# Kernel tuning notes

Measured on AMD Instinct MI355X. Metric: run time of the kernel, lower is better.

## Reference

```python
import jax, jax.numpy as jnp
import numpy as np

EPS = 1e-05


def setup_inputs() -> dict:
    key = jax.random.key(0)
    k1, k2, k3, k4 = jax.random.split(key, 4)
    B, N, L, J = 1, 256, 192, 32
    n_feat_out = 128
    d2 = J * J  # 1024
    x_down = jax.random.normal(k1, (B, N, L, J), dtype=jnp.float32)
    x_down_w = jax.random.normal(k2, (B, N, L, J), dtype=jnp.float32)
    a_2 = jnp.ones((d2,), dtype=jnp.float32)
    b_2 = jnp.zeros((d2,), dtype=jnp.float32)
    # nn.Linear default init: U(-1/sqrt(fan_in), 1/sqrt(fan_in))
    bound = 1.0 / np.sqrt(d2)
    W = jax.random.uniform(k3, (d2, n_feat_out), dtype=jnp.float32, minval=-bound, maxval=bound)
    b = jax.random.uniform(k4, (n_feat_out,), dtype=jnp.float32, minval=-bound, maxval=bound)
    return {"x_down": x_down, "x_down_w": x_down_w, "a_2": a_2, "b_2": b_2, "W": W, "b": b}


def reference(x_down, x_down_w, a_2, b_2, W, b):
    B, N, L, J = x_down.shape
    # outer-product contraction over MSA dim: (B,L,L,J,J)
    pair = jnp.einsum('bnij,bnlm->biljm', x_down, x_down_w)
    pair = pair.reshape(B, L, L, J * J)
    # LayerNorm over last dim (biased variance, matching torch unbiased=False)
    mean = pair.mean(axis=-1, keepdims=True)
    var = pair.var(axis=-1, keepdims=True)
    pair = a_2 * (pair - mean) / jnp.sqrt(var + EPS) + b_2
    # Linear projection J^2 -> n_feat_out
    return pair @ W + b
```

## Files before the change

kernel.cpp:

```cpp
#include <hip/hip_runtime.h>
#include <hip/hip_bf16.h>
#include <stdint.h>

#define NN   256
#define LL   192
#define MDIM 6144
#define D2   1024
#define FF   128

typedef __bf16 bf16x8 __attribute__((ext_vector_type(8)));
typedef float  f32x4  __attribute__((ext_vector_type(4)));

#define MFMA16(a, b, c) __builtin_amdgcn_mfma_f32_16x16x32_bf16(a, b, c, 0, 0, 0)

__device__ __forceinline__ void gload_lds16(const void* g, void* l) {
  __builtin_amdgcn_global_load_lds(
      (__attribute__((address_space(1))) void*)(g),
      (__attribute__((address_space(3))) void*)(l),
      16, 0, 0);
}

static __device__ __forceinline__ unsigned short bf16_bits(float v) {
  __bf16 h = (__bf16)v;
  return __builtin_bit_cast(unsigned short, h);
}

__global__ __launch_bounds__(256)
void prep_all(const float* __restrict__ x1, const float* __restrict__ x2,
              const float* __restrict__ W, const float* __restrict__ a2,
              const float* __restrict__ b2, const float* __restrict__ bias,
              __bf16* __restrict__ At, __bf16* __restrict__ Bt,
              __bf16* __restrict__ WB, float* __restrict__ S,
              float* __restrict__ T) {
  __shared__ float tile[64][65];
  const int b = blockIdx.x;
  const int t = threadIdx.x;
  if (b < 768) {
    const float* src = (b < 384) ? x1 : x2;
    __bf16* dst = (b < 384) ? At : Bt;
    const int bb = (b < 384) ? b : b - 384;
    const int m0 = (bb % 96) * 64;
    const int k0 = (bb / 96) * 64;
    const int rr = t >> 4;
    const int cc = (t & 15) * 4;
#pragma unroll
    for (int it = 0; it < 4; ++it) {
      const int kr = rr + it * 16;
      const float4 v = *(const float4*)&src[(size_t)(k0 + kr) * MDIM + m0 + cc];
      tile[kr][cc + 0] = v.x;
      tile[kr][cc + 1] = v.y;
      tile[kr][cc + 2] = v.z;
      tile[kr][cc + 3] = v.w;
    }
    __syncthreads();
#pragma unroll
    for (int it = 0; it < 4; ++it) {
      const int mr = rr + it * 16;
      ushort4 u;
      u.x = bf16_bits(tile[cc + 0][mr]);
      u.y = bf16_bits(tile[cc + 1][mr]);
      u.z = bf16_bits(tile[cc + 2][mr]);
      u.w = bf16_bits(tile[cc + 3][mr]);
      *(ushort4*)&dst[(size_t)(m0 + mr) * NN + k0 + cc] = u;
    }
  } else {
    const int f = b - 768;
    float s = 0.f, tt = 0.f;
#pragma unroll
    for (int it = 0; it < 4; ++it) {
      const int k = t + it * 256;
      const float wv = W[(size_t)k * FF + f];
      const __bf16 wa = (__bf16)(a2[k] * wv);
      WB[(size_t)(k >> 5) * 4096 + f * 32 + ((k >> 3) & 3) * 8 + (k & 7)] = wa;
      s += (float)wa;
      tt += b2[k] * wv;
    }
#pragma unroll
    for (int off = 32; off; off >>= 1) {
      s += __shfl_xor(s, off);
      tt += __shfl_xor(tt, off);
    }
    const int wv_ = t >> 6, ln = t & 63;
    if (ln == 0) { tile[0][wv_] = s; tile[1][wv_] = tt; }
    __syncthreads();
    if (t == 0) {
      S[f] = tile[0][0] + tile[0][1] + tile[0][2] + tile[0][3];
      T[f] = tile[1][0] + tile[1][1] + tile[1][2] + tile[1][3] + bias[f];
    }
  }
}

__global__ __launch_bounds__(512, 4)
void fused10(const __bf16* __restrict__ At, const __bf16* __restrict__ Bt,
             const __bf16* __restrict__ WB, const float* __restrict__ S,
             const float* __restrict__ T, float* __restrict__ out) {
  __shared__ uint8_t lds[65536];
  __shared__ float mean_s[32], rstd_s[32];

  const int tid = threadIdx.x;
  const int w = tid >> 6;
  const int lane = tid & 63;
  const int q = lane >> 4;
  const int c = lane & 15;

  const int b = blockIdx.x;
  const int xcd = b & 7;
  const int s_ = b >> 3;
  const int bx = (xcd >> 1) * 12 + (s_ % 12);
  const int by = (xcd & 1) * 12 + (s_ / 12);
  const int m0 = bx * 128, n0 = by * 256;

  uint8_t* As = lds;
  uint8_t* Bs = lds + 16384;

  const int l8 = lane & 7;
  const int r8 = lane >> 3;
  const int gsw = l8 ^ r8;

  f32x4 acc[4][4];
#pragma unroll
  for (int i = 0; i < 4; ++i)
#pragma unroll
    for (int j = 0; j < 4; ++j)
      acc[i][j] = (f32x4){0.f, 0.f, 0.f, 0.f};

  const int mbase = (w & 1) * 64;
  const int nbase = (w >> 1) * 64;

  {
    const __bf16* gA = At + (size_t)(m0 + w * 16 + r8) * NN + gsw * 8;
    const __bf16* gB = Bt + (size_t)(n0 + w * 32 + r8) * NN + gsw * 8;
#pragma unroll 1
    for (int kb = 0; kb < 4; ++kb) {
      __syncthreads();
#pragma unroll
      for (int j = 0; j < 2; ++j)
        gload_lds16(gA + (size_t)j * 8 * NN, As + (w * 16 + j * 8) * 128);
#pragma unroll
      for (int j = 0; j < 4; ++j)
        gload_lds16(gB + (size_t)j * 8 * NN, Bs + (w * 32 + j * 8) * 128);
      __syncthreads();
#pragma unroll
      for (int ks = 0; ks < 2; ++ks) {
        const int slot = ((ks * 4 + q) ^ (lane & 7)) * 16;
        bf16x8 a[4];
#pragma unroll
        for (int t4 = 0; t4 < 4; ++t4)
          a[t4] = *(const bf16x8*)(As + (mbase + t4 * 16 + c) * 128 + slot);
#pragma unroll
        for (int tj = 0; tj < 4; ++tj) {
          const bf16x8 bfr =
              *(const bf16x8*)(Bs + (nbase + tj * 16 + c) * 128 + slot);
#pragma unroll
          for (int ti = 0; ti < 4; ++ti)
            acc[ti][tj] = MFMA16(a[ti], bfr, acc[ti][tj]);
        }
      }
      gA += 64;
      gB += 64;
    }
  }

  const int fs = w * 16;
  const __bf16* wbp = WB + (fs + c) * 32 + q * 8;
  bf16x8 pb[8];
  pb[0] = *(const bf16x8*)(wbp);
  pb[1] = *(const bf16x8*)(wbp + 4096);

  __syncthreads();

  const int i_hi = w & 1, l_hi = w >> 1;
#pragma unroll
  for (int ab = 0; ab < 2; ++ab) {
#pragma unroll
    for (int cb = 0; cb < 2; ++cb) {
      float s1 = 0.f, s2 = 0.f;
#pragma unroll
      for (int dti = 0; dti < 2; ++dti)
#pragma unroll
        for (int dtj = 0; dtj < 2; ++dtj)
#pragma unroll
          for (int reg = 0; reg < 4; ++reg) {
            const float v = acc[ab * 2 + dti][cb * 2 + dtj][reg];
            s1 += v; s2 += v * v;
          }
#pragma unroll
      for (int off = 32; off; off >>= 1) {
        s1 += __shfl_xor(s1, off);
        s2 += __shfl_xor(s2, off);
      }
      const float mean = s1 * (1.0f / 1024.0f);
      const float var = s2 * (1.0f / 1024.0f) - mean * mean;
      const float rstd = rsqrtf(var + 1e-5f);
      const int r = (i_hi * 2 + ab) * 8 + l_hi * 2 + cb;
      if (lane == 0) { mean_s[r] = mean; rstd_s[r] = rstd; }
      const int r7 = r & 7;
#pragma unroll
      for (int dti = 0; dti < 2; ++dti)
#pragma unroll
        for (int dtj = 0; dtj < 2; ++dtj)
#pragma unroll
          for (int rp = 0; rp < 4; rp += 2) {
            const float x = acc[ab * 2 + dti][cb * 2 + dtj][rp];
            const float y = acc[ab * 2 + dti][cb * 2 + dtj][rp + 1];
            const float send = (c & 1) ? x : y;
            const float recv = __shfl_xor(send, 1);
            const float vlo = (c & 1) ? recv : x;
            const float vhi = (c & 1) ? y : recv;
            const int reg_w = (c & 1) ? rp + 1 : rp;
            const int j = dti * 16 + q * 4 + reg_w;
            const int mm0 = dtj * 16 + (c & ~1);
            const int k = j * 32 + mm0;
            const int g = k >> 3;
            const int G = g ^ (g >> 4) ^ r7;
            const uint32_t dw =
                ((uint32_t)bf16_bits(vhi) << 16) | (uint32_t)bf16_bits(vlo);
            *(uint32_t*)(lds + r * 2048 + G * 16 + (mm0 & 7) * 2) = dw;
          }
    }
  }

  __syncthreads();
  __builtin_amdgcn_sched_barrier(0);

#pragma unroll
  for (int p = 2; p < 8; ++p)
    pb[p] = *(const bf16x8*)(wbp + p * 4096);

  f32x4 acc2[2];
  acc2[0] = (f32x4){0.f, 0.f, 0.f, 0.f};
  acc2[1] = (f32x4){0.f, 0.f, 0.f, 0.f};
  const int c7 = c & 7;
#pragma unroll
  for (int kstep = 0; kstep < 32; ++kstep) {
    const int g = kstep * 4 + q;
    const int G = g ^ (g >> 4) ^ c7;
    const bf16x8 a0 = *(const bf16x8*)(lds + c * 2048 + G * 16);
    const bf16x8 a1 = *(const bf16x8*)(lds + (16 + c) * 2048 + G * 16);
    acc2[0] = MFMA16(a0, pb[kstep & 7], acc2[0]);
    acc2[1] = MFMA16(a1, pb[kstep & 7], acc2[1]);
    if (kstep < 24)
      pb[kstep & 7] = *(const bf16x8*)(wbp + (kstep + 8) * 4096);
  }

  const float S0 = S[fs + c], T0 = T[fs + c];
#pragma unroll
  for (int reg = 0; reg < 4; ++reg) {
    const int r0 = q * 4 + reg;
    const int r1 = 16 + r0;
    {
      const float mean = mean_s[r0], rstd = rstd_s[r0];
      const int i = bx * 4 + (r0 >> 3);
      const int l = by * 8 + (r0 & 7);
      out[((size_t)i * LL + l) * FF + fs + c] =
          rstd * (acc2[0][reg] - mean * S0) + T0;
    }
    {
      const float mean = mean_s[r1], rstd = rstd_s[r1];
      const int i = bx * 4 + (r1 >> 3);
      const int l = by * 8 + (r1 & 7);
      out[((size_t)i * LL + l) * FF + fs + c] =
          rstd * (acc2[1][reg] - mean * S0) + T0;
    }
  }
}

extern "C" void kernel_launch(void* const* d_in, const int* in_sizes, int n_in,
                              void* d_out, int out_size, void* d_ws, size_t ws_size,
                              hipStream_t stream) {
  const float* x_down   = (const float*)d_in[0];
  const float* x_down_w = (const float*)d_in[1];
  const float* a2       = (const float*)d_in[2];
  const float* b2       = (const float*)d_in[3];
  const float* W        = (const float*)d_in[4];
  const float* bias     = (const float*)d_in[5];
  float* out = (float*)d_out;

  uint8_t* ws = (uint8_t*)d_ws;
  __bf16* At  = (__bf16*)(ws);
  __bf16* Bt  = (__bf16*)(ws + 3145728);
  __bf16* WB  = (__bf16*)(ws + 6291456);
  float*  S   = (float*)(ws + 6553600);
  float*  T   = (float*)(ws + 6554112);

  prep_all<<<dim3(896), dim3(256), 0, stream>>>(x_down, x_down_w, W, a2, b2,
                                                bias, At, Bt, WB, S, T);
  fused10<<<dim3(1152), dim3(512), 0, stream>>>(At, Bt, WB, S, T, out);
}
```

Baseline: 123.6 us.

## Load B fragments directly to registers and give each wave an 8x2 MFMA tile

Each wave now owns a 128x32 output slice (8x2 MFMA tiles) instead of 64x64. Its B operand is loaded straight from global memory into registers, while only A still goes through LDS. This drops the B LDS staging and its reads. In exchange each wave makes more A reads from LDS, and the B global loads are no longer swizzled or coalesced as before. The LayerNorm epilogue is remapped so each wave reduces a full pair row over its two tiles.

Result: slower. 131.9 us (+6.7%).

```diff
diff --git a/kernel.cpp b/kernel.cpp
--- a/kernel.cpp
+++ b/kernel.cpp
@@ -91,7 +91,7 @@
 }
 
 __global__ __launch_bounds__(512, 4)
-void fused10(const __bf16* __restrict__ At, const __bf16* __restrict__ Bt,
+void fused15(const __bf16* __restrict__ At, const __bf16* __restrict__ Bt,
              const __bf16* __restrict__ WB, const float* __restrict__ S,
              const float* __restrict__ T, float* __restrict__ out) {
   __shared__ uint8_t lds[65536];
@@ -111,53 +111,48 @@
   const int m0 = bx * 128, n0 = by * 256;
 
   uint8_t* As = lds;
-  uint8_t* Bs = lds + 16384;
 
   const int l8 = lane & 7;
   const int r8 = lane >> 3;
   const int gsw = l8 ^ r8;
 
-  f32x4 acc[4][4];
-#pragma unroll
-  for (int i = 0; i < 4; ++i)
-#pragma unroll
-    for (int j = 0; j < 4; ++j)
-      acc[i][j] = (f32x4){0.f, 0.f, 0.f, 0.f};
-
-  const int mbase = (w & 1) * 64;
-  const int nbase = (w >> 1) * 64;
+  f32x4 acc[8][2];
+#pragma unroll
+  for (int i = 0; i < 8; ++i) {
+    acc[i][0] = (f32x4){0.f, 0.f, 0.f, 0.f};
+    acc[i][1] = (f32x4){0.f, 0.f, 0.f, 0.f};
+  }
 
   {
     const __bf16* gA = At + (size_t)(m0 + w * 16 + r8) * NN + gsw * 8;
-    const __bf16* gB = Bt + (size_t)(n0 + w * 32 + r8) * NN + gsw * 8;
+    const __bf16* gB0 = Bt + (size_t)(n0 + w * 32 + c) * NN + q * 8;
+    const __bf16* gB1 = gB0 + (size_t)16 * NN;
 #pragma unroll 1
     for (int kb = 0; kb < 4; ++kb) {
       __syncthreads();
-#pragma unroll
-      for (int j = 0; j < 2; ++j)
-        gload_lds16(gA + (size_t)j * 8 * NN, As + (w * 16 + j * 8) * 128);
-#pragma unroll
-      for (int j = 0; j < 4; ++j)
-        gload_lds16(gB + (size_t)j * 8 * NN, Bs + (w * 32 + j * 8) * 128);
+      gload_lds16(gA, As + (w * 16) * 128);
+      gload_lds16(gA + (size_t)8 * NN, As + (w * 16 + 8) * 128);
+      const bf16x8 b00 = *(const bf16x8*)(gB0);
+      const bf16x8 b01 = *(const bf16x8*)(gB1);
+      const bf16x8 b10 = *(const bf16x8*)(gB0 + 32);
+      const bf16x8 b11 = *(const bf16x8*)(gB1 + 32);
+      __builtin_amdgcn_sched_barrier(0);
       __syncthreads();
 #pragma unroll
       for (int ks = 0; ks < 2; ++ks) {
-        const int slot = ((ks * 4 + q) ^ (lane & 7)) * 16;
-        bf16x8 a[4];
-#pragma unroll
-        for (int t4 = 0; t4 < 4; ++t4)
-          a[t4] = *(const bf16x8*)(As + (mbase + t4 * 16 + c) * 128 + slot);
-#pragma unroll
-        for (int tj = 0; tj < 4; ++tj) {
-          const bf16x8 bfr =
-              *(const bf16x8*)(Bs + (nbase + tj * 16 + c) * 128 + slot);
-#pragma unroll
-          for (int ti = 0; ti < 4; ++ti)
-            acc[ti][tj] = MFMA16(a[ti], bfr, acc[ti][tj]);
+        const bf16x8 bk0 = ks ? b10 : b00;
+        const bf16x8 bk1 = ks ? b11 : b01;
+        const int slot = ((ks * 4 + q) ^ l8) * 16;
+#pragma unroll
+        for (int t8 = 0; t8 < 8; ++t8) {
+          const bf16x8 a = *(const bf16x8*)(As + (t8 * 16 + c) * 128 + slot);
+          acc[t8][0] = MFMA16(a, bk0, acc[t8][0]);
+          acc[t8][1] = MFMA16(a, bk1, acc[t8][1]);
         }
       }
       gA += 64;
-      gB += 64;
+      gB0 += 64;
+      gB1 += 64;
     }
   }
 
@@ -169,55 +164,51 @@
 
   __syncthreads();
 
-  const int i_hi = w & 1, l_hi = w >> 1;
-#pragma unroll
-  for (int ab = 0; ab < 2; ++ab) {
-#pragma unroll
-    for (int cb = 0; cb < 2; ++cb) {
-      float s1 = 0.f, s2 = 0.f;
-#pragma unroll
-      for (int dti = 0; dti < 2; ++dti)
-#pragma unroll
-        for (int dtj = 0; dtj < 2; ++dtj)
-#pragma unroll
-          for (int reg = 0; reg < 4; ++reg) {
-            const float v = acc[ab * 2 + dti][cb * 2 + dtj][reg];
-            s1 += v; s2 += v * v;
-          }
-#pragma unroll
-      for (int off = 32; off; off >>= 1) {
-        s1 += __shfl_xor(s1, off);
-        s2 += __shfl_xor(s2, off);
-      }
-      const float mean = s1 * (1.0f / 1024.0f);
-      const float var = s2 * (1.0f / 1024.0f) - mean * mean;
-      const float rstd = rsqrtf(var + 1e-5f);
-      const int r = (i_hi * 2 + ab) * 8 + l_hi * 2 + cb;
-      if (lane == 0) { mean_s[r] = mean; rstd_s[r] = rstd; }
-      const int r7 = r & 7;
-#pragma unroll
-      for (int dti = 0; dti < 2; ++dti)
-#pragma unroll
-        for (int dtj = 0; dtj < 2; ++dtj)
-#pragma unroll
-          for (int rp = 0; rp < 4; rp += 2) {
-            const float x = acc[ab * 2 + dti][cb * 2 + dtj][rp];
-            const float y = acc[ab * 2 + dti][cb * 2 + dtj][rp + 1];
-            const float send = (c & 1) ? x : y;
-            const float recv = __shfl_xor(send, 1);
-            const float vlo = (c & 1) ? recv : x;
-            const float vhi = (c & 1) ? y : recv;
-            const int reg_w = (c & 1) ? rp + 1 : rp;
-            const int j = dti * 16 + q * 4 + reg_w;
-            const int mm0 = dtj * 16 + (c & ~1);
-            const int k = j * 32 + mm0;
-            const int g = k >> 3;
-            const int G = g ^ (g >> 4) ^ r7;
-            const uint32_t dw =
-                ((uint32_t)bf16_bits(vhi) << 16) | (uint32_t)bf16_bits(vlo);
-            *(uint32_t*)(lds + r * 2048 + G * 16 + (mm0 & 7) * 2) = dw;
-          }
-    }
+#pragma unroll
+  for (int rp4 = 0; rp4 < 4; ++rp4) {
+    float s1 = 0.f, s2 = 0.f;
+#pragma unroll
+    for (int th = 0; th < 2; ++th)
+#pragma unroll
+      for (int tj = 0; tj < 2; ++tj)
+#pragma unroll
+        for (int reg = 0; reg < 4; ++reg) {
+          const float v = acc[rp4 * 2 + th][tj][reg];
+          s1 += v; s2 += v * v;
+        }
+#pragma unroll
+    for (int off = 32; off; off >>= 1) {
+      s1 += __shfl_xor(s1, off);
+      s2 += __shfl_xor(s2, off);
+    }
+    const float mean = s1 * (1.0f / 1024.0f);
+    const float var = s2 * (1.0f / 1024.0f) - mean * mean;
+    const float rstd = rsqrtf(var + 1e-5f);
+    const int r = rp4 * 8 + w;
+    if (lane == 0) { mean_s[r] = mean; rstd_s[r] = rstd; }
+    const int r7 = r & 7;
+#pragma unroll
+    for (int th = 0; th < 2; ++th)
+#pragma unroll
+      for (int tj = 0; tj < 2; ++tj)
+#pragma unroll
+        for (int rp = 0; rp < 4; rp += 2) {
+          const float x = acc[rp4 * 2 + th][tj][rp];
+          const float y = acc[rp4 * 2 + th][tj][rp + 1];
+          const float send = (c & 1) ? x : y;
+          const float recv = __shfl_xor(send, 1);
+          const float vlo = (c & 1) ? recv : x;
+          const float vhi = (c & 1) ? y : recv;
+          const int reg_w = (c & 1) ? rp + 1 : rp;
+          const int j = th * 16 + q * 4 + reg_w;
+          const int mm0 = tj * 16 + (c & ~1);
+          const int k = j * 32 + mm0;
+          const int g = k >> 3;
+          const int G = g ^ (g >> 4) ^ r7;
+          const uint32_t dw =
+              ((uint32_t)bf16_bits(vhi) << 16) | (uint32_t)bf16_bits(vlo);
+          *(uint32_t*)(lds + r * 2048 + G * 16 + (mm0 & 7) * 2) = dw;
+        }
   }
 
   __syncthreads();
@@ -285,5 +276,5 @@
 
   prep_all<<<dim3(896), dim3(256), 0, stream>>>(x_down, x_down_w, W, a2, b2,
                                                 bias, At, Bt, WB, S, T);
-  fused10<<<dim3(1152), dim3(512), 0, stream>>>(At, Bt, WB, S, T, out);
-}
+  fused15<<<dim3(1152), dim3(512), 0, stream>>>(At, Bt, WB, S, T, out);
+}
```
